# Optimization experiments

Hardware: AMD Instinct MI355X
Metric: run time of the kernel (lower is better)

The kernel has to match this reference:

```python
import jax, jax.numpy as jnp
import numpy as np

B, T, D = 4, 2048, 2048
H, DK, DV = 16, 128, 128


def setup_inputs() -> dict:
    key = jax.random.key(0)
    ks = jax.random.split(key, 8)
    s = 1.0 / np.sqrt(D)
    return {
        "q": jax.random.normal(ks[0], (B, T, D), jnp.float32),
        "k": jax.random.normal(ks[1], (B, T, D), jnp.float32),
        "v": jax.random.normal(ks[2], (B, T, D), jnp.float32),
        "mask": jnp.tril(jnp.ones((T, T), dtype=bool)),  # True = attend
        # weights stored as [in, out] (torch Linear applies x @ W.T)
        "Wq": jax.random.normal(ks[3], (D, H * DK), jnp.float32) * s,
        "Wk": jax.random.normal(ks[4], (D, H * DK), jnp.float32) * s,
        "Wv": jax.random.normal(ks[5], (D, H * DV), jnp.float32) * s,
        "Wo": jax.random.normal(ks[6], (H * DV, D), jnp.float32) * s,
    }


def _attention(q, k, v, mask, Wq, Wk, Wv, Wo):
    # project and split heads: [B,T,H*dh] -> [B,H,T,dh]
    def split_heads(x, dh):
        b, t, _ = x.shape
        return x.reshape(b, t, H, dh).transpose(0, 2, 1, 3)

    q_i = split_heads(q @ Wq, DK)
    k_i = split_heads(k @ Wk, DK)
    v_i = split_heads(v @ Wv, DV)

    scores = jnp.einsum("bhik,bhjk->bhij", q_i, k_i) / jnp.sqrt(
        jnp.asarray(DK, q_i.dtype)
    )
    neg = -jnp.finfo(scores.dtype).max
    scores = jnp.where(mask[None, None, :, :], scores, neg)
    attn = jax.nn.softmax(scores, axis=-1)
    vals = jnp.einsum("bhij,bhjv->bhiv", attn, v_i)  # [B,H,T,dv]
    merged = vals.transpose(0, 2, 1, 3).reshape(q.shape[0], q.shape[1], H * DV)
    return merged @ Wo


def reference(q, k, v, mask, Wq, Wk, Wv, Wo):
    return _attention(q, k, v, mask, Wq, Wk, Wv, Wo)
```

## Files before the change

### kernel.cpp

```cpp
#include <hip/hip_runtime.h>
#include <hip/hip_bf16.h>

typedef __attribute__((ext_vector_type(8))) short bf16x8;
typedef __attribute__((ext_vector_type(4))) unsigned short u16x4;
typedef __attribute__((ext_vector_type(4))) float f32x4;

constexpr int Bb = 4, Tt = 2048, Dd = 2048, Hh = 16, DHd = 128;

static __device__ __forceinline__ unsigned short f2bf(float f) {
  union { float f; unsigned u; } x; x.f = f;
  unsigned r = x.u + 0x7fffu + ((x.u >> 16) & 1u);
  return (unsigned short)(r >> 16);
}

static __device__ __forceinline__ void gld16(const void* g, void* l) {
  __builtin_amdgcn_global_load_lds(
      (__attribute__((address_space(1))) void*)g,
      (__attribute__((address_space(3))) void*)l, 16, 0, 0);
}

__global__ __launch_bounds__(256) void cvt_bf16(const float* __restrict__ s,
                                                unsigned short* __restrict__ d) {
  const size_t i = ((size_t)blockIdx.x * 256 + threadIdx.x) * 8;
  float4 a = *(const float4*)(s + i);
  float4 b = *(const float4*)(s + i + 4);
  bf16x8 pk;
  pk[0] = (short)f2bf(a.x); pk[1] = (short)f2bf(a.y);
  pk[2] = (short)f2bf(a.z); pk[3] = (short)f2bf(a.w);
  pk[4] = (short)f2bf(b.x); pk[5] = (short)f2bf(b.y);
  pk[6] = (short)f2bf(b.z); pk[7] = (short)f2bf(b.w);
  *(bf16x8*)(d + i) = pk;
}

__global__ __launch_bounds__(256) void wtrans_all(
    const float* __restrict__ Wq, const float* __restrict__ Wk,
    const float* __restrict__ Wv, const float* __restrict__ Wo,
    unsigned short* __restrict__ WqT, unsigned short* __restrict__ WkT,
    unsigned short* __restrict__ WvT, unsigned short* __restrict__ WoT,
    float qscale) {
  __shared__ __align__(16) unsigned short tile[64][72];
  const float* src;
  unsigned short* dst;
  float sc = 1.0f;
  switch (blockIdx.z) {
    case 0: src = Wq; dst = WqT; sc = qscale; break;
    case 1: src = Wk; dst = WkT; break;
    case 2: src = Wv; dst = WvT; break;
    default: src = Wo; dst = WoT; break;
  }
  const int t = threadIdx.x;
  const int k0 = blockIdx.x * 64, n0 = blockIdx.y * 64;
  const int c = t & 15, r = t >> 4;
#pragma unroll
  for (int p = 0; p < 4; ++p) {
    const int rr = r + 16 * p;
    float4 v = *(const float4*)(src + (size_t)(k0 + rr) * Dd + n0 + c * 4);
    u16x4 pk;
    pk[0] = f2bf(v.x * sc); pk[1] = f2bf(v.y * sc);
    pk[2] = f2bf(v.z * sc); pk[3] = f2bf(v.w * sc);
    *(u16x4*)&tile[rr][c * 4] = pk;
  }
  __syncthreads();
#pragma unroll
  for (int p = 0; p < 4; ++p) {
    const int nn = r + 16 * p;
    u16x4 pk;
    pk[0] = tile[c * 4 + 0][nn]; pk[1] = tile[c * 4 + 1][nn];
    pk[2] = tile[c * 4 + 2][nn]; pk[3] = tile[c * 4 + 3][nn];
    *(u16x4*)(dst + (size_t)(n0 + nn) * Dd + k0 + c * 4) = pk;
  }
}

template <int OMODE>
__global__ __launch_bounds__(256, 2) void gemm_bt(
    const unsigned short* __restrict__ A, const unsigned short* __restrict__ Bt,
    void* __restrict__ Outp) {
  __shared__ __align__(16) unsigned short As[128 * 64];
  __shared__ __align__(16) unsigned short Bs[128 * 64];
  const int t = threadIdx.x;
  const int lane = t & 63, w = t >> 6;
  const int wr = w >> 1, wc = w & 1;
  const int fr = lane & 15, fq = lane >> 4;
  const int m0 = blockIdx.x * 128, n0 = blockIdx.y * 128;
  const int srow = t >> 3, scol = (t & 7) * 8;
  const unsigned short* Ag = A + (size_t)(m0 + srow) * Dd + scol;
  const unsigned short* Bg = Bt + (size_t)(n0 + srow) * Dd + scol;
  unsigned short* Asl = As + t * 8;
  unsigned short* Bsl = Bs + t * 8;

  f32x4 acc[4][4] = {};

  for (int k0 = 0; k0 < Dd; k0 += 64) {
#pragma unroll
    for (int i = 0; i < 4; ++i) {
      gld16(Ag + (size_t)i * 32 * Dd + k0, Asl + i * 2048);
      gld16(Bg + (size_t)i * 32 * Dd + k0, Bsl + i * 2048);
    }
    __syncthreads();
#pragma unroll
    for (int ks = 0; ks < 2; ++ks) {
      bf16x8 af[4], bfr[4];
#pragma unroll
      for (int m = 0; m < 4; ++m)
        af[m] = *(const bf16x8*)&As[(wr * 64 + m * 16 + fr) * 64 + ks * 32 + fq * 8];
#pragma unroll
      for (int n = 0; n < 4; ++n)
        bfr[n] = *(const bf16x8*)&Bs[(wc * 64 + n * 16 + fr) * 64 + ks * 32 + fq * 8];
#pragma unroll
      for (int m = 0; m < 4; ++m)
#pragma unroll
        for (int n = 0; n < 4; ++n)
          acc[m][n] = __builtin_amdgcn_mfma_f32_16x16x32_bf16(
              af[m], bfr[n], acc[m][n], 0, 0, 0);
    }
    __syncthreads();
  }

#pragma unroll
  for (int m = 0; m < 4; ++m) {
    const int mg = m0 + wr * 64 + m * 16 + fq * 4;
    const int bb = mg >> 11, tt0 = mg & (Tt - 1);
#pragma unroll
    for (int n = 0; n < 4; ++n) {
      const int ng = n0 + wc * 64 + n * 16 + fr;
      if (OMODE == 0) {
        float* o = (float*)Outp + (size_t)mg * Dd + ng;
#pragma unroll
        for (int r = 0; r < 4; ++r) o[(size_t)r * Dd] = acc[m][n][r];
      } else if (OMODE == 1) {
        const int h = ng >> 7, dh = ng & 127;
        unsigned short* o = (unsigned short*)Outp +
                            (((size_t)bb * Hh + h) * Tt + tt0) * DHd + dh;
#pragma unroll
        for (int r = 0; r < 4; ++r) o[r * DHd] = f2bf(acc[m][n][r]);
      } else {
        const int h = ng >> 7, dh = ng & 127;
        u16x4 pk;
#pragma unroll
        for (int r = 0; r < 4; ++r) pk[r] = f2bf(acc[m][n][r]);
        *(u16x4*)((unsigned short*)Outp +
                  (((size_t)bb * Hh + h) * DHd + dh) * Tt + tt0) = pk;
      }
    }
  }
}

__global__ __launch_bounds__(256, 2) void fattn(
    const unsigned short* __restrict__ Qp, const unsigned short* __restrict__ Kp,
    const unsigned short* __restrict__ Vt, unsigned short* __restrict__ Ao) {
  __shared__ __align__(16) unsigned short Ks[2][64 * 128];
  __shared__ __align__(16) unsigned short Vs[2][128 * 64];
  const int t = threadIdx.x, lane = t & 63, w = t >> 6;
  const int fr = lane & 15, fq = lane >> 4;
  const int rsw = fr & 7;
  const int id = blockIdx.x;
  const int xcd = id & 7, slot = id >> 3;
  const int bh = xcd * 8 + (slot >> 4);
  const int qb = 15 - (slot & 15);
  const int q0w = qb * 128 + w * 32;
  const unsigned short* Qb = Qp + (size_t)bh * Tt * DHd;
  const unsigned short* Kb = Kp + (size_t)bh * Tt * DHd;
  const unsigned short* Vb = Vt + (size_t)bh * DHd * Tt;

  bf16x8 qf[2][4];
#pragma unroll
  for (int mg = 0; mg < 2; ++mg)
#pragma unroll
    for (int ks = 0; ks < 4; ++ks)
      qf[mg][ks] = *(const bf16x8*)(Qb + (size_t)(q0w + mg * 16 + fr) * DHd +
                                    ks * 32 + fq * 8);

  f32x4 oacc[2][8] = {};
  float m_[2] = {-1e30f, -1e30f};
  float l_[2] = {0.f, 0.f};

  auto STAGE = [&](int b, int kv0) {
#pragma unroll
    for (int p = 0; p < 4; ++p) {
      const int idx = t + p * 256, row = idx >> 4, ch = idx & 15;
      gld16(Kb + (size_t)(kv0 + row) * DHd + ((ch ^ (row & 7)) * 8),
            &Ks[b][idx * 8]);
    }
#pragma unroll
    for (int p = 0; p < 4; ++p) {
      const int idx = t + p * 256, row = idx >> 3, ch = idx & 7;
      gld16(Vb + (size_t)row * Tt + kv0 + ((ch ^ (row & 7)) * 8),
            &Vs[b][idx * 8]);
    }
  };

  const int ntile = 2 * qb + 2;
  STAGE(0, 0);
  int cur = 0;

  for (int kt = 0; kt < ntile; ++kt) {
    const int kv0 = kt * 64;
    __builtin_amdgcn_s_barrier();
    if (kt + 1 < ntile) {
      STAGE(cur ^ 1, (kt + 1) * 64);
      asm volatile("s_waitcnt vmcnt(8)" ::: "memory");
    } else {
      asm volatile("s_waitcnt vmcnt(0)" ::: "memory");
    }
    __builtin_amdgcn_sched_barrier(0);
    __builtin_amdgcn_s_barrier();

    if (kv0 <= q0w + 31) {
      const unsigned short* Kc = &Ks[cur][0];
      const unsigned short* Vc = &Vs[cur][0];

      f32x4 s[2][4] = {};
      __builtin_amdgcn_s_setprio(1);
#pragma unroll
      for (int tt = 0; tt < 4; ++tt) {
        bf16x8 kf[4];
#pragma unroll
        for (int ks = 0; ks < 4; ++ks)
          kf[ks] = *(const bf16x8*)(Kc + (tt * 16 + fr) * 128 +
                                    ((ks * 4 + fq) ^ rsw) * 8);
#pragma unroll
        for (int ks = 0; ks < 4; ++ks) {
          s[0][tt] = __builtin_amdgcn_mfma_f32_16x16x32_bf16(kf[ks], qf[0][ks],
                                                             s[0][tt], 0, 0, 0);
          s[1][tt] = __builtin_amdgcn_mfma_f32_16x16x32_bf16(kf[ks], qf[1][ks],
                                                             s[1][tt], 0, 0, 0);
        }
      }
      __builtin_amdgcn_s_setprio(0);

      uint2 c[2][4];
#pragma unroll
      for (int mg = 0; mg < 2; ++mg) {
        const int qg = q0w + mg * 16;
        if (kv0 + 63 > qg) {
          const int qa = qg + fr;
#pragma unroll
          for (int tt = 0; tt < 4; ++tt)
#pragma unroll
            for (int r = 0; r < 4; ++r)
              if (kv0 + tt * 16 + fq * 4 + r > qa) s[mg][tt][r] = -1e30f;
        }

        float tmax = s[mg][0][0];
#pragma unroll
        for (int tt = 0; tt < 4; ++tt)
#pragma unroll
          for (int r = 0; r < 4; ++r) tmax = fmaxf(tmax, s[mg][tt][r]);
        tmax = fmaxf(tmax, __shfl_xor(tmax, 16));
        tmax = fmaxf(tmax, __shfl_xor(tmax, 32));

        if (!__all(tmax <= m_[mg] + 8.0f)) {
          const float mn = fmaxf(m_[mg], tmax);
          const float alpha = __builtin_amdgcn_exp2f(m_[mg] - mn);
          m_[mg] = mn;
          float al4[4];
#pragma unroll
          for (int r = 0; r < 4; ++r) al4[r] = __shfl(alpha, fq * 4 + r);
#pragma unroll
          for (int dt = 0; dt < 8; ++dt)
#pragma unroll
            for (int r = 0; r < 4; ++r) oacc[mg][dt][r] *= al4[r];
          l_[mg] *= alpha;
        }

        float rs = 0.f;
#pragma unroll
        for (int tt = 0; tt < 4; ++tt)
#pragma unroll
          for (int r = 0; r < 4; ++r) {
            const float p = __builtin_amdgcn_exp2f(s[mg][tt][r] - m_[mg]);
            s[mg][tt][r] = p;
            rs += p;
          }
        rs += __shfl_xor(rs, 16);
        rs += __shfl_xor(rs, 32);
        l_[mg] += rs;

#pragma unroll
        for (int tt = 0; tt < 4; ++tt) {
          unsigned r0, r1;
          asm("v_cvt_pk_bf16_f32 %0, %1, %2"
              : "=v"(r0) : "v"(s[mg][tt][0]), "v"(s[mg][tt][1]));
          asm("v_cvt_pk_bf16_f32 %0, %1, %2"
              : "=v"(r1) : "v"(s[mg][tt][2]), "v"(s[mg][tt][3]));
          c[mg][tt].x = r0; c[mg][tt].y = r1;
        }
      }

      const int src0 = fr + 32 * (fq & 1);
      const int src1 = src0 + 16;
      const bool hi = (fq >> 1) != 0;
      __builtin_amdgcn_s_setprio(1);
#pragma unroll
      for (int ks2 = 0; ks2 < 2; ++ks2) {
        bf16x8 pf[2];
#pragma unroll
        for (int mg = 0; mg < 2; ++mg) {
          const int a0 = __shfl((int)c[mg][2 * ks2].x, src0);
          const int b0 = __shfl((int)c[mg][2 * ks2 + 1].x, src0);
          const int a1 = __shfl((int)c[mg][2 * ks2].y, src0);
          const int b1 = __shfl((int)c[mg][2 * ks2 + 1].y, src0);
          const int a2 = __shfl((int)c[mg][2 * ks2].x, src1);
          const int b2 = __shfl((int)c[mg][2 * ks2 + 1].x, src1);
          const int a3 = __shfl((int)c[mg][2 * ks2].y, src1);
          const int b3 = __shfl((int)c[mg][2 * ks2 + 1].y, src1);
          union { int wd[4]; bf16x8 v; } pu;
          pu.wd[0] = hi ? b0 : a0;
          pu.wd[1] = hi ? b1 : a1;
          pu.wd[2] = hi ? b2 : a2;
          pu.wd[3] = hi ? b3 : a3;
          pf[mg] = pu.v;
        }
#pragma unroll
        for (int dt = 0; dt < 8; ++dt) {
          const bf16x8 vf = *(const bf16x8*)(Vc + (dt * 16 + fr) * 64 +
                                             ((ks2 * 4 + fq) ^ rsw) * 8);
          oacc[0][dt] = __builtin_amdgcn_mfma_f32_16x16x32_bf16(pf[0], vf,
                                                                oacc[0][dt], 0, 0, 0);
          oacc[1][dt] = __builtin_amdgcn_mfma_f32_16x16x32_bf16(pf[1], vf,
                                                                oacc[1][dt], 0, 0, 0);
        }
      }
      __builtin_amdgcn_s_setprio(0);
    }
    cur ^= 1;
  }

  const int bb = bh >> 4, hh = bh & 15;
#pragma unroll
  for (int mg = 0; mg < 2; ++mg) {
    float linv[4];
#pragma unroll
    for (int r = 0; r < 4; ++r) linv[r] = 1.0f / __shfl(l_[mg], fq * 4 + r);
    const int qrow = q0w + mg * 16 + fq * 4;
#pragma unroll
    for (int r = 0; r < 4; ++r) {
      unsigned short* o = Ao + ((size_t)bb * Tt + qrow + r) * Dd + hh * DHd + fr;
#pragma unroll
      for (int dt = 0; dt < 8; ++dt) o[dt * 16] = f2bf(oacc[mg][dt][r] * linv[r]);
    }
  }
}

extern "C" void kernel_launch(void* const* d_in, const int* in_sizes, int n_in,
                              void* d_out, int out_size, void* d_ws, size_t ws_size,
                              hipStream_t stream) {
  const float* q = (const float*)d_in[0];
  const float* k = (const float*)d_in[1];
  const float* v = (const float*)d_in[2];
  const float* Wq = (const float*)d_in[4];
  const float* Wk = (const float*)d_in[5];
  const float* Wv = (const float*)d_in[6];
  const float* Wo = (const float*)d_in[7];

  const size_t WE = (size_t)Dd * Dd;
  const size_t PE = (size_t)Bb * Hh * Tt * DHd;
  unsigned short* WqT = (unsigned short*)d_ws;
  unsigned short* WkT = WqT + WE;
  unsigned short* WvT = WkT + WE;
  unsigned short* WoT = WvT + WE;
  unsigned short* Qx = WoT + WE;
  unsigned short* Kx = Qx + PE;
  unsigned short* Vx = Kx + PE;
  unsigned short* Ax = Vx + PE;

  const float qscale = (float)(1.4426950408889634 / 11.313708498984761);
  wtrans_all<<<dim3(32, 32, 4), 256, 0, stream>>>(
      Wq, Wk, Wv, Wo, WqT, WkT, WvT, WoT, qscale);

  cvt_bf16<<<dim3(8192), 256, 0, stream>>>(q, Ax);
  gemm_bt<1><<<dim3(64, 16), 256, 0, stream>>>(Ax, WqT, Qx);
  cvt_bf16<<<dim3(8192), 256, 0, stream>>>(k, Ax);
  gemm_bt<1><<<dim3(64, 16), 256, 0, stream>>>(Ax, WkT, Kx);
  cvt_bf16<<<dim3(8192), 256, 0, stream>>>(v, Ax);
  gemm_bt<2><<<dim3(64, 16), 256, 0, stream>>>(Ax, WvT, Vx);
  fattn<<<dim3(1024), 256, 0, stream>>>(Qx, Kx, Vx, Ax);
  gemm_bt<0><<<dim3(64, 16), 256, 0, stream>>>(Ax, WoT, (float*)d_out);
}
```

Baseline: 549.3 us.

## Replace projection GEMM with 256x256 tile, 4-stage async LDS pipeline kernel

Replaces the 128x128 single-buffered projection GEMM with a 512-thread 256x256 tile kernel. It streams 32-wide K slices through a 4-deep LDS ring using global_load_lds, with explicit vmcnt waits and raw barriers so loads overlap MFMA work. It also raises priority around the MFMA block and remaps block order so neighbouring blocks share tiles in cache. The costs are 128KB of LDS per block, more accumulator registers, and only 256 blocks per GEMM, which may underfill the device's CUs.

```diff
diff --git a/kernel.cpp b/kernel.cpp
--- a/kernel.cpp
+++ b/kernel.cpp
@@ -72,57 +72,83 @@
 }
 
 template <int OMODE>
-__global__ __launch_bounds__(256, 2) void gemm_bt(
+__global__ __launch_bounds__(512, 2) void gemm256(
     const unsigned short* __restrict__ A, const unsigned short* __restrict__ Bt,
     void* __restrict__ Outp) {
-  __shared__ __align__(16) unsigned short As[128 * 64];
-  __shared__ __align__(16) unsigned short Bs[128 * 64];
-  const int t = threadIdx.x;
-  const int lane = t & 63, w = t >> 6;
-  const int wr = w >> 1, wc = w & 1;
+  __shared__ __align__(16) unsigned short As[4 * 8192];
+  __shared__ __align__(16) unsigned short Bs[4 * 8192];
+  const int t = threadIdx.x, lane = t & 63, w = t >> 6;
+  const int wm = w >> 2, wn = w & 3;
   const int fr = lane & 15, fq = lane >> 4;
-  const int m0 = blockIdx.x * 128, n0 = blockIdx.y * 128;
-  const int srow = t >> 3, scol = (t & 7) * 8;
-  const unsigned short* Ag = A + (size_t)(m0 + srow) * Dd + scol;
-  const unsigned short* Bg = Bt + (size_t)(n0 + srow) * Dd + scol;
-  unsigned short* Asl = As + t * 8;
-  unsigned short* Bsl = Bs + t * 8;
-
-  f32x4 acc[4][4] = {};
-
-  for (int k0 = 0; k0 < Dd; k0 += 64) {
-#pragma unroll
-    for (int i = 0; i < 4; ++i) {
-      gld16(Ag + (size_t)i * 32 * Dd + k0, Asl + i * 2048);
-      gld16(Bg + (size_t)i * 32 * Dd + k0, Bsl + i * 2048);
-    }
-    __syncthreads();
-#pragma unroll
-    for (int ks = 0; ks < 2; ++ks) {
-      bf16x8 af[4], bfr[4];
-#pragma unroll
-      for (int m = 0; m < 4; ++m)
-        af[m] = *(const bf16x8*)&As[(wr * 64 + m * 16 + fr) * 64 + ks * 32 + fq * 8];
+  const int slot = blockIdx.x;
+  const int orig = (slot & 7) * 32 + (slot >> 3);
+  const int m0 = (orig >> 3) * 256, n0 = (orig & 7) * 256;
+
+  f32x4 acc[8][4] = {};
+  const int aoff = (wm * 128 + fr) * 32 + fq * 8;
+  const int boff = (wn * 64 + fr) * 32 + fq * 8;
+
+  auto STAGE = [&](int kt) {
+    const int b = kt & 3;
+    const int k0 = kt * 32;
+#pragma unroll
+    for (int p = 0; p < 2; ++p) {
+      const int idx = t + p * 512, row = idx >> 2, ch = idx & 3;
+      gld16(A + (size_t)(m0 + row) * Dd + k0 + ch * 8, &As[b * 8192 + idx * 8]);
+    }
+#pragma unroll
+    for (int p = 0; p < 2; ++p) {
+      const int idx = t + p * 512, row = idx >> 2, ch = idx & 3;
+      gld16(Bt + (size_t)(n0 + row) * Dd + k0 + ch * 8, &Bs[b * 8192 + idx * 8]);
+    }
+  };
+
+  constexpr int NT = Dd / 32;
+  STAGE(0); STAGE(1); STAGE(2);
+
+  for (int kt = 0; kt < NT; ++kt) {
+    if (kt + 3 < NT) {
+      STAGE(kt + 3);
+      asm volatile("s_waitcnt vmcnt(12)" ::: "memory");
+    } else if (kt + 2 < NT) {
+      asm volatile("s_waitcnt vmcnt(8)" ::: "memory");
+    } else if (kt + 1 < NT) {
+      asm volatile("s_waitcnt vmcnt(4)" ::: "memory");
+    } else {
+      asm volatile("s_waitcnt vmcnt(0)" ::: "memory");
+    }
+    __builtin_amdgcn_sched_barrier(0);
+    __builtin_amdgcn_s_barrier();
+    __builtin_amdgcn_sched_barrier(0);
+
+    const int bo = (kt & 3) * 8192;
+    bf16x8 af[8], bf[4];
+#pragma unroll
+    for (int m = 0; m < 8; ++m)
+      af[m] = *(const bf16x8*)&As[bo + aoff + m * 512];
+#pragma unroll
+    for (int n = 0; n < 4; ++n)
+      bf[n] = *(const bf16x8*)&Bs[bo + boff + n * 512];
+
+    __builtin_amdgcn_s_setprio(1);
+#pragma unroll
+    for (int m = 0; m < 8; ++m)
 #pragma unroll
       for (int n = 0; n < 4; ++n)
-        bfr[n] = *(const bf16x8*)&Bs[(wc * 64 + n * 16 + fr) * 64 + ks * 32 + fq * 8];
-#pragma unroll
-      for (int m = 0; m < 4; ++m)
-#pragma unroll
-        for (int n = 0; n < 4; ++n)
-          acc[m][n] = __builtin_amdgcn_mfma_f32_16x16x32_bf16(
-              af[m], bfr[n], acc[m][n], 0, 0, 0);
-    }
-    __syncthreads();
-  }
-
-#pragma unroll
-  for (int m = 0; m < 4; ++m) {
-    const int mg = m0 + wr * 64 + m * 16 + fq * 4;
+        acc[m][n] = __builtin_amdgcn_mfma_f32_16x16x32_bf16(af[m], bf[n],
+                                                            acc[m][n], 0, 0, 0);
+    __builtin_amdgcn_s_setprio(0);
+    __builtin_amdgcn_sched_barrier(0);
+    __builtin_amdgcn_s_barrier();
+  }
+
+#pragma unroll
+  for (int m = 0; m < 8; ++m) {
+    const int mg = m0 + wm * 128 + m * 16 + fq * 4;
     const int bb = mg >> 11, tt0 = mg & (Tt - 1);
 #pragma unroll
     for (int n = 0; n < 4; ++n) {
-      const int ng = n0 + wc * 64 + n * 16 + fr;
+      const int ng = n0 + wn * 64 + n * 16 + fr;
       if (OMODE == 0) {
         float* o = (float*)Outp + (size_t)mg * Dd + ng;
 #pragma unroll
@@ -369,11 +395,11 @@
       Wq, Wk, Wv, Wo, WqT, WkT, WvT, WoT, qscale);
 
   cvt_bf16<<<dim3(8192), 256, 0, stream>>>(q, Ax);
-  gemm_bt<1><<<dim3(64, 16), 256, 0, stream>>>(Ax, WqT, Qx);
+  gemm256<1><<<dim3(256), 512, 0, stream>>>(Ax, WqT, Qx);
   cvt_bf16<<<dim3(8192), 256, 0, stream>>>(k, Ax);
-  gemm_bt<1><<<dim3(64, 16), 256, 0, stream>>>(Ax, WkT, Kx);
+  gemm256<1><<<dim3(256), 512, 0, stream>>>(Ax, WkT, Kx);
   cvt_bf16<<<dim3(8192), 256, 0, stream>>>(v, Ax);
-  gemm_bt<2><<<dim3(64, 16), 256, 0, stream>>>(Ax, WvT, Vx);
+  gemm256<2><<<dim3(256), 512, 0, stream>>>(Ax, WvT, Vx);
   fattn<<<dim3(1024), 256, 0, stream>>>(Qx, Kx, Vx, Ax);
-  gemm_bt<0><<<dim3(64, 16), 256, 0, stream>>>(Ax, WoT, (float*)d_out);
-}
+  gemm256<0><<<dim3(256), 512, 0, stream>>>(Ax, WoT, (float*)d_out);
+}
```

After: 584.0 us. 1.06x slower.
